# Kernel tuning notes

Hardware: AMD Instinct MI355X
Metric: run time of the kernel (lower is better)

The kernel has to match this reference:

```python
import jax, jax.numpy as jnp
import numpy as np

N_NODES = 50000
N_EDGES = 800000
HIDDEN = 100
NUM_TASKS = 128
NUM_GRAPHS = 2000
ATOM_DIMS = [119, 5, 12, 12, 10, 6, 6, 2, 2]  # OGB full_atom_feature_dims
EPS = 1e-16  # stands in for PyG's clamp(min=0) so that pow(-1) stays finite


def setup_inputs() -> dict:
    key = jax.random.key(0)
    ks = jax.random.split(key, 8)
    x = jax.random.randint(ks[0], (N_NODES, 9), 0, 2, dtype=jnp.int32)
    edge_index = jax.random.randint(ks[1], (2, N_EDGES), 0, N_NODES, dtype=jnp.int32)
    batch = jnp.sort(jax.random.randint(ks[2], (N_NODES,), 0, NUM_GRAPHS, dtype=jnp.int32))
    s = 1.0 / np.sqrt(HIDDEN)
    atom_emb = jax.random.normal(ks[3], (sum(ATOM_DIMS), HIDDEN), jnp.float32)
    W1 = jax.random.normal(ks[4], (HIDDEN, HIDDEN), jnp.float32) * s
    b1 = jnp.zeros((HIDDEN,), jnp.float32)
    W2 = jax.random.normal(ks[5], (HIDDEN, HIDDEN), jnp.float32) * s
    b2 = jnp.zeros((HIDDEN,), jnp.float32)
    Wlin = jax.random.normal(ks[6], (HIDDEN, NUM_TASKS), jnp.float32) * s
    blin = jnp.zeros((NUM_TASKS,), jnp.float32)
    return dict(x=x, edge_index=edge_index, batch=batch, atom_emb=atom_emb,
                W1=W1, b1=b1, W2=W2, b2=b2, Wlin=Wlin, blin=blin)


def reference(x, edge_index, batch, atom_emb, W1, b1, W2, b2, Wlin, blin):
    # --- AtomEncoder: sum of per-feature categorical embeddings ---
    offsets = jnp.asarray(np.concatenate([[0], np.cumsum(ATOM_DIMS)[:-1]]), jnp.int32)
    h = jnp.take(atom_emb, x + offsets[None, :], axis=0).sum(axis=1)  # [N, H]

    # --- GCN normalization with self-loops (gcn_norm, edge_weight=None) ---
    loops = jnp.arange(N_NODES, dtype=edge_index.dtype)
    row = jnp.concatenate([edge_index[0], loops])  # source
    col = jnp.concatenate([edge_index[1], loops])  # target
    ew = jnp.ones(row.shape[0], jnp.float32)
    deg = jax.ops.segment_sum(ew, col, num_segments=N_NODES)  # in-degree incl self-loop
    dinv = jnp.where(deg > 0, deg ** -0.5, 0.0)
    norm = dinv[row] * ew * dinv[col]  # [E+N]
    cnt = jnp.maximum(deg, 1.0)  # messages per target node (for mean)

    def gcn_conv(h, W, b):
        msg = norm[:, None] * (h @ W)[row]  # [E+N, H]
        # PowerMeanAggregation(p=-1): clamp(0,100).pow(-1) -> mean -> clamp(0,100).pow(-1)
        msg = jnp.clip(msg, EPS, 100.0) ** (-1.0)
        agg = jax.ops.segment_sum(msg, col, num_segments=N_NODES) / cnt[:, None]
        return jnp.clip(agg, EPS, 100.0) ** (-1.0) + b

    h = jax.nn.relu(gcn_conv(h, W1, b1))
    h = gcn_conv(h, W2, b2)

    # --- global_mean_pool over batch ---
    gcnt = jax.ops.segment_sum(jnp.ones((N_NODES,), jnp.float32), batch, num_segments=NUM_GRAPHS)
    pooled = jax.ops.segment_sum(h, batch, num_segments=NUM_GRAPHS) / jnp.maximum(gcnt, 1.0)[:, None]

    return pooled @ Wlin + blin  # [NUM_GRAPHS, NUM_TASKS]
```

## Files before the change

### kernel.cpp

```cpp
#include <hip/hip_runtime.h>

#define N_NODES   50000
#define N_EDGES   800000
#define HIDDEN    100
#define NUM_TASKS 128
#define NUM_GRAPHS 2000
#define EPS 1e-16f

static __device__ __forceinline__ float rcp_fast(float v) {
    return __builtin_amdgcn_rcpf(v);
}
static __device__ __forceinline__ float invclip(float v) {
    return rcp_fast(fminf(fmaxf(v, EPS), 100.0f));
}
static __device__ __forceinline__ unsigned pack_bf16x2(float a, float b) {
    unsigned r;
    asm("v_cvt_pk_bf16_f32 %0, %1, %2" : "=v"(r) : "v"(a), "v"(b));
    return r;
}

__global__ void deg_count_kernel(const int* __restrict__ col, int* __restrict__ deg) {
    int e = blockIdx.x * blockDim.x + threadIdx.x;
    if (e < N_EDGES) atomicAdd(&deg[col[e]], 1);
}

__global__ void blk_sum_kernel(const int* __restrict__ deg, int* __restrict__ bsum) {
    int i = blockIdx.x * 256 + threadIdx.x;
    int v = (i < N_NODES) ? deg[i] : 0;
#pragma unroll
    for (int off = 32; off > 0; off >>= 1) v += __shfl_down(v, off, 64);
    __shared__ int ws[4];
    if ((threadIdx.x & 63) == 0) ws[threadIdx.x >> 6] = v;
    __syncthreads();
    if (threadIdx.x == 0) bsum[blockIdx.x] = ws[0] + ws[1] + ws[2] + ws[3];
}

__global__ void bsum_scan_kernel(int* __restrict__ bsum, int nblk) {
    __shared__ int buf[256];
    int t = threadIdx.x;
    int v = (t < nblk) ? bsum[t] : 0;
    buf[t] = v;
    __syncthreads();
    for (int off = 1; off < 256; off <<= 1) {
        int x = (t >= off) ? buf[t - off] : 0;
        __syncthreads();
        buf[t] += x;
        __syncthreads();
    }
    if (t < nblk) bsum[t] = buf[t] - v;
}

__global__ void blk_scan_kernel(const int* __restrict__ deg, const int* __restrict__ bbase,
                                int* __restrict__ csr_off, float* __restrict__ dinv,
                                int* __restrict__ cursor) {
    __shared__ int buf[256];
    int t = threadIdx.x;
    int i = blockIdx.x * 256 + t;
    int dv = (i < N_NODES) ? deg[i] : 0;
    buf[t] = dv;
    __syncthreads();
    for (int off = 1; off < 256; off <<= 1) {
        int x = (t >= off) ? buf[t - off] : 0;
        __syncthreads();
        buf[t] += x;
        __syncthreads();
    }
    if (i < N_NODES) {
        csr_off[i] = bbase[blockIdx.x] + buf[t] - dv;
        dinv[i] = 1.0f / sqrtf((float)(dv + 1));
        cursor[i] = 0;
    } else if (i == N_NODES) {
        csr_off[N_NODES] = N_EDGES;
    }
}

__global__ void scatter_kernel(const int* __restrict__ row, const int* __restrict__ col,
                               const int* __restrict__ csr_off, int* __restrict__ cursor,
                               const float* __restrict__ dinv, int2* __restrict__ csr_pack) {
    int e = blockIdx.x * blockDim.x + threadIdx.x;
    if (e >= N_EDGES) return;
    int s = row[e], d = col[e];
    int pos = csr_off[d] + atomicAdd(&cursor[d], 1);
    int2 p;
    p.x = s;
    p.y = __float_as_int(dinv[s] * dinv[d]);
    csr_pack[pos] = p;
}

__global__ void encoder_kernel(const int* __restrict__ x, const float* __restrict__ emb,
                               float* __restrict__ h) {
    int n = blockIdx.x;
    int d = threadIdx.x;
    if (d >= HIDDEN) return;
    const int offs[9] = {0, 119, 124, 136, 148, 158, 164, 170, 172};
    float acc = 0.0f;
#pragma unroll
    for (int f = 0; f < 9; ++f) {
        int idx = x[n * 9 + f] + offs[f];
        acc += emb[idx * HIDDEN + d];
    }
    h[n * HIDDEN + d] = acc;
}

#define MM_NODES 64
#define WL_PAD   10032
__global__ __launch_bounds__(512) void matmul_kernel(const float* __restrict__ h,
                                                     const float* __restrict__ W,
                                                     unsigned* __restrict__ outb) {
    __shared__ float Wl[WL_PAD];
    __shared__ float hl[MM_NODES * HIDDEN];
    int tid = threadIdx.x;
    int nb = blockIdx.x * MM_NODES;

    for (int i = tid; i < WL_PAD; i += 512)
        Wl[i] = (i < HIDDEN * HIDDEN) ? W[i] : 0.0f;
    for (int i = tid; i < MM_NODES * HIDDEN; i += 512) {
        int n = i / HIDDEN;
        hl[i] = (nb + n < N_NODES) ? h[(size_t)(nb + n) * HIDDEN + (i % HIDDEN)] : 0.0f;
    }
    __syncthreads();

    int tx = tid & 31;
    int ty = tid >> 5;

    float4 acc[4];
#pragma unroll
    for (int jn = 0; jn < 4; ++jn) acc[jn] = make_float4(0.f, 0.f, 0.f, 0.f);

    for (int kk = 0; kk < HIDDEN; kk += 4) {
        float hs[4][4];
#pragma unroll
        for (int jn = 0; jn < 4; ++jn) {
            float4 hv = *(const float4*)&hl[(ty + 16 * jn) * HIDDEN + kk];
            hs[jn][0] = hv.x; hs[jn][1] = hv.y; hs[jn][2] = hv.z; hs[jn][3] = hv.w;
        }
#pragma unroll
        for (int dk = 0; dk < 4; ++dk) {
            float4 wv = *(const float4*)&Wl[(kk + dk) * HIDDEN + 4 * tx];
#pragma unroll
            for (int jn = 0; jn < 4; ++jn) {
                acc[jn].x += hs[jn][dk] * wv.x;
                acc[jn].y += hs[jn][dk] * wv.y;
                acc[jn].z += hs[jn][dk] * wv.z;
                acc[jn].w += hs[jn][dk] * wv.w;
            }
        }
    }

    if (tx < 25) {
#pragma unroll
        for (int jn = 0; jn < 4; ++jn) {
            int n = nb + ty + 16 * jn;
            if (n < N_NODES) {
                uint2 pk;
                pk.x = pack_bf16x2(acc[jn].x, acc[jn].y);
                pk.y = pack_bf16x2(acc[jn].z, acc[jn].w);
                *(uint2*)&outb[(size_t)n * 50 + 2 * tx] = pk;
            }
        }
    }
}

__global__ __launch_bounds__(128) void agg_kernel(
        const unsigned* __restrict__ hw16, const int* __restrict__ csr_off,
        const int2* __restrict__ csr_pack, const float* __restrict__ dinv,
        const int* __restrict__ deg, const float* __restrict__ bias,
        float* __restrict__ out, int relu) {
    int wid  = (blockIdx.x * blockDim.x + threadIdx.x) >> 6;
    int lane = threadIdx.x & 63;
    if (wid >= N_NODES) return;
    int n = wid;
    bool act = lane < 50;

    float cnt = (float)(deg[n] + 1);
    float dn  = dinv[n];
    float nrm = dn * dn;

    float2 acc = make_float2(0.f, 0.f);
    if (act) {
        unsigned u = hw16[(size_t)n * 50 + lane];
        acc.x = invclip(nrm * __int_as_float(u << 16));
        acc.y = invclip(nrm * __int_as_float(u & 0xFFFF0000u));
    }

    int beg = csr_off[n], end = csr_off[n + 1];
    int i = beg;
    for (; i + 4 <= end; i += 4) {
        int2 p0 = csr_pack[i];
        int2 p1 = csr_pack[i + 1];
        int2 p2 = csr_pack[i + 2];
        int2 p3 = csr_pack[i + 3];
        unsigned u0 = act ? hw16[(size_t)p0.x * 50 + lane] : 0u;
        unsigned u1 = act ? hw16[(size_t)p1.x * 50 + lane] : 0u;
        unsigned u2 = act ? hw16[(size_t)p2.x * 50 + lane] : 0u;
        unsigned u3 = act ? hw16[(size_t)p3.x * 50 + lane] : 0u;
        float w0 = __int_as_float(p0.y), w1 = __int_as_float(p1.y);
        float w2 = __int_as_float(p2.y), w3 = __int_as_float(p3.y);
        acc.x += invclip(w0 * __int_as_float(u0 << 16));
        acc.y += invclip(w0 * __int_as_float(u0 & 0xFFFF0000u));
        acc.x += invclip(w1 * __int_as_float(u1 << 16));
        acc.y += invclip(w1 * __int_as_float(u1 & 0xFFFF0000u));
        acc.x += invclip(w2 * __int_as_float(u2 << 16));
        acc.y += invclip(w2 * __int_as_float(u2 & 0xFFFF0000u));
        acc.x += invclip(w3 * __int_as_float(u3 << 16));
        acc.y += invclip(w3 * __int_as_float(u3 & 0xFFFF0000u));
    }
    for (; i < end; ++i) {
        int2 p = csr_pack[i];
        unsigned u = act ? hw16[(size_t)p.x * 50 + lane] : 0u;
        float w = __int_as_float(p.y);
        acc.x += invclip(w * __int_as_float(u << 16));
        acc.y += invclip(w * __int_as_float(u & 0xFFFF0000u));
    }

    if (act) {
        float rcnt = rcp_fast(cnt);
        float2 o;
        o.x = invclip(acc.x * rcnt) + bias[2 * lane];
        o.y = invclip(acc.y * rcnt) + bias[2 * lane + 1];
        if (relu) { o.x = fmaxf(o.x, 0.f); o.y = fmaxf(o.y, 0.f); }
        *(float2*)&out[(size_t)n * HIDDEN + 2 * lane] = o;
    }
}

__global__ void pool_final_kernel(const float* __restrict__ h, const int* __restrict__ batch,
                                  const float* __restrict__ Wlin, const float* __restrict__ blin,
                                  float* __restrict__ out) {
    int g = blockIdx.x;
    int t = threadIdx.x;
    __shared__ float pl[HIDDEN];

    int lo = 0, hi = N_NODES;
    while (lo < hi) { int mid = (lo + hi) >> 1; if (batch[mid] < g) lo = mid + 1; else hi = mid; }
    int start = lo;
    hi = N_NODES;
    while (lo < hi) { int mid = (lo + hi) >> 1; if (batch[mid] < g + 1) lo = mid + 1; else hi = mid; }
    int end = lo;

    float inv = 1.0f / fmaxf((float)(end - start), 1.0f);
    if (t < HIDDEN) {
        float acc = 0.f;
        for (int n = start; n < end; ++n) acc += h[(size_t)n * HIDDEN + t];
        pl[t] = acc * inv;
    }
    __syncthreads();

    float o = 0.f;
#pragma unroll 4
    for (int j = 0; j < HIDDEN; ++j) o += pl[j] * Wlin[j * NUM_TASKS + t];
    out[(size_t)g * NUM_TASKS + t] = o + blin[t];
}

extern "C" void kernel_launch(void* const* d_in, const int* in_sizes, int n_in,
                              void* d_out, int out_size, void* d_ws, size_t ws_size,
                              hipStream_t stream) {
    const int*   x     = (const int*)d_in[0];
    const int*   ei    = (const int*)d_in[1];
    const int*   batch = (const int*)d_in[2];
    const float* emb   = (const float*)d_in[3];
    const float* W1    = (const float*)d_in[4];
    const float* b1    = (const float*)d_in[5];
    const float* W2    = (const float*)d_in[6];
    const float* b2    = (const float*)d_in[7];
    const float* Wlin  = (const float*)d_in[8];
    const float* blin  = (const float*)d_in[9];
    float* out = (float*)d_out;

    const int* row = ei;
    const int* col = ei + N_EDGES;

    char* ws = (char*)d_ws;
    auto alloc = [&](size_t bytes) -> char* {
        char* p = ws;
        ws += (bytes + 255) & ~(size_t)255;
        return p;
    };
    int*      deg      = (int*)     alloc((size_t)N_NODES * 4);
    int*      cursor   = (int*)     alloc((size_t)N_NODES * 4);
    int*      csr_off  = (int*)     alloc((size_t)(N_NODES + 1) * 4);
    float*    dinv     = (float*)   alloc((size_t)N_NODES * 4);
    int2*     csr_pack = (int2*)    alloc((size_t)N_EDGES * 8);
    float*    bufA     = (float*)   alloc((size_t)N_NODES * HIDDEN * 4);
    unsigned* hw16     = (unsigned*)alloc((size_t)N_NODES * 50 * 4);
    int*      bsum     = (int*)     alloc(256 * 4);

    const int SCAN_BLOCKS = (N_NODES + 255) / 256;

    hipMemsetAsync(deg, 0, (size_t)N_NODES * 4, stream);
    deg_count_kernel<<<(N_EDGES + 255) / 256, 256, 0, stream>>>(col, deg);
    blk_sum_kernel<<<SCAN_BLOCKS, 256, 0, stream>>>(deg, bsum);
    bsum_scan_kernel<<<1, 256, 0, stream>>>(bsum, SCAN_BLOCKS);
    blk_scan_kernel<<<SCAN_BLOCKS, 256, 0, stream>>>(deg, bsum, csr_off, dinv, cursor);
    scatter_kernel<<<(N_EDGES + 255) / 256, 256, 0, stream>>>(row, col, csr_off, cursor, dinv,
                                                              csr_pack);
    encoder_kernel<<<N_NODES, 128, 0, stream>>>(x, emb, bufA);

    const int MM_BLOCKS = (N_NODES + MM_NODES - 1) / MM_NODES;
    matmul_kernel<<<MM_BLOCKS, 512, 0, stream>>>(bufA, W1, hw16);
    agg_kernel<<<(N_NODES + 1) / 2, 128, 0, stream>>>(hw16, csr_off, csr_pack,
                                                      dinv, deg, b1, bufA, 1);
    matmul_kernel<<<MM_BLOCKS, 512, 0, stream>>>(bufA, W2, hw16);
    agg_kernel<<<(N_NODES + 1) / 2, 128, 0, stream>>>(hw16, csr_off, csr_pack,
                                                      dinv, deg, b2, bufA, 0);

    pool_final_kernel<<<NUM_GRAPHS, 128, 0, stream>>>(bufA, batch, Wlin, blin, out);
}
```

Before: 317.5 us.

## Process two nodes per wavefront in aggregation with 8-byte bf16 gathers

The aggregation kernel now maps two destination nodes onto each 64-lane wavefront, one per half-wave. Each of 25 active lanes per half loads a uint2 holding four bf16 features, so 50 of 64 lanes do work instead of 50 of 64 with 4-byte loads. The goal is fewer wavefronts, wider memory transactions and better lane use. The cost is divergence: the edge loop runs until both halves finish, so the wave follows the higher-degree node, and out-of-range neighbour slots load clamped indices.

```diff
diff --git a/kernel.cpp b/kernel.cpp
--- a/kernel.cpp
+++ b/kernel.cpp
@@ -18,6 +18,8 @@
     asm("v_cvt_pk_bf16_f32 %0, %1, %2" : "=v"(r) : "v"(a), "v"(b));
     return r;
 }
+static __device__ __forceinline__ float bf_lo(unsigned u) { return __int_as_float(u << 16); }
+static __device__ __forceinline__ float bf_hi(unsigned u) { return __int_as_float(u & 0xFFFF0000u); }
 
 __global__ void deg_count_kernel(const int* __restrict__ col, int* __restrict__ deg) {
     int e = blockIdx.x * blockDim.x + threadIdx.x;
@@ -161,65 +163,67 @@
     }
 }
 
-__global__ __launch_bounds__(128) void agg_kernel(
+__global__ __launch_bounds__(256) void agg_kernel(
         const unsigned* __restrict__ hw16, const int* __restrict__ csr_off,
         const int2* __restrict__ csr_pack, const float* __restrict__ dinv,
         const int* __restrict__ deg, const float* __restrict__ bias,
         float* __restrict__ out, int relu) {
     int wid  = (blockIdx.x * blockDim.x + threadIdx.x) >> 6;
     int lane = threadIdx.x & 63;
-    if (wid >= N_NODES) return;
-    int n = wid;
-    bool act = lane < 50;
+    if (wid >= (N_NODES + 1) / 2) return;
+    int half = lane >> 5;
+    int q    = lane & 31;
+    int n    = 2 * wid + half;
+    bool act = q < 25;
+
+    const uint2* hw2 = (const uint2*)hw16;
 
     float cnt = (float)(deg[n] + 1);
     float dn  = dinv[n];
     float nrm = dn * dn;
 
-    float2 acc = make_float2(0.f, 0.f);
+    float a0 = 0.f, a1 = 0.f, a2 = 0.f, a3 = 0.f;
     if (act) {
-        unsigned u = hw16[(size_t)n * 50 + lane];
-        acc.x = invclip(nrm * __int_as_float(u << 16));
-        acc.y = invclip(nrm * __int_as_float(u & 0xFFFF0000u));
-    }
-
-    int beg = csr_off[n], end = csr_off[n + 1];
-    int i = beg;
-    for (; i + 4 <= end; i += 4) {
-        int2 p0 = csr_pack[i];
-        int2 p1 = csr_pack[i + 1];
-        int2 p2 = csr_pack[i + 2];
-        int2 p3 = csr_pack[i + 3];
-        unsigned u0 = act ? hw16[(size_t)p0.x * 50 + lane] : 0u;
-        unsigned u1 = act ? hw16[(size_t)p1.x * 50 + lane] : 0u;
-        unsigned u2 = act ? hw16[(size_t)p2.x * 50 + lane] : 0u;
-        unsigned u3 = act ? hw16[(size_t)p3.x * 50 + lane] : 0u;
-        float w0 = __int_as_float(p0.y), w1 = __int_as_float(p1.y);
-        float w2 = __int_as_float(p2.y), w3 = __int_as_float(p3.y);
-        acc.x += invclip(w0 * __int_as_float(u0 << 16));
-        acc.y += invclip(w0 * __int_as_float(u0 & 0xFFFF0000u));
-        acc.x += invclip(w1 * __int_as_float(u1 << 16));
-        acc.y += invclip(w1 * __int_as_float(u1 & 0xFFFF0000u));
-        acc.x += invclip(w2 * __int_as_float(u2 << 16));
-        acc.y += invclip(w2 * __int_as_float(u2 & 0xFFFF0000u));
-        acc.x += invclip(w3 * __int_as_float(u3 << 16));
-        acc.y += invclip(w3 * __int_as_float(u3 & 0xFFFF0000u));
-    }
-    for (; i < end; ++i) {
-        int2 p = csr_pack[i];
-        unsigned u = act ? hw16[(size_t)p.x * 50 + lane] : 0u;
-        float w = __int_as_float(p.y);
-        acc.x += invclip(w * __int_as_float(u << 16));
-        acc.y += invclip(w * __int_as_float(u & 0xFFFF0000u));
+        uint2 u = hw2[(size_t)n * 25 + q];
+        a0 = invclip(nrm * bf_lo(u.x)); a1 = invclip(nrm * bf_hi(u.x));
+        a2 = invclip(nrm * bf_lo(u.y)); a3 = invclip(nrm * bf_hi(u.y));
+    }
+
+    int beg = csr_off[n];
+    int len = csr_off[n + 1] - beg;
+
+    const long long* packs = (const long long*)csr_pack;
+    for (int k = 0; __any(k < len); k += 4) {
+#pragma unroll
+        for (int j = 0; j < 4; ++j) {
+            int kk = k + j;
+            bool on = kk < len;
+            int idx = beg + (on ? kk : (len > 0 ? len - 1 : 0));
+            idx = (idx < N_EDGES) ? idx : (N_EDGES - 1);
+            long long qp = packs[idx];
+            int   src = (int)qp;
+            float w   = __int_as_float((int)(qp >> 32));
+            if (on & act) {
+                uint2 u = hw2[(size_t)src * 25 + q];
+                a0 += invclip(w * bf_lo(u.x)); a1 += invclip(w * bf_hi(u.x));
+                a2 += invclip(w * bf_lo(u.y)); a3 += invclip(w * bf_hi(u.y));
+            }
+        }
     }
 
     if (act) {
         float rcnt = rcp_fast(cnt);
-        float2 o;
-        o.x = invclip(acc.x * rcnt) + bias[2 * lane];
-        o.y = invclip(acc.y * rcnt) + bias[2 * lane + 1];
-        if (relu) { o.x = fmaxf(o.x, 0.f); o.y = fmaxf(o.y, 0.f); }
-        *(float2*)&out[(size_t)n * HIDDEN + 2 * lane] = o;
+        float4 bv = *(const float4*)&bias[4 * q];
+        float4 o;
+        o.x = invclip(a0 * rcnt) + bv.x;
+        o.y = invclip(a1 * rcnt) + bv.y;
+        o.z = invclip(a2 * rcnt) + bv.z;
+        o.w = invclip(a3 * rcnt) + bv.w;
+        if (relu) {
+            o.x = fmaxf(o.x, 0.f); o.y = fmaxf(o.y, 0.f);
+            o.z = fmaxf(o.z, 0.f); o.w = fmaxf(o.w, 0.f);
+        }
+        *(float4*)&out[(size_t)n * HIDDEN + 4 * q] = o;
     }
 }
 
@@ -295,13 +299,16 @@
                                                               csr_pack);
     encoder_kernel<<<N_NODES, 128, 0, stream>>>(x, emb, bufA);
 
-    const int MM_BLOCKS = (N_NODES + MM_NODES - 1) / MM_NODES;
+    const int MM_BLOCKS  = (N_NODES + MM_NODES - 1) / MM_NODES;
+    const int AGG_WAVES  = (N_NODES + 1) / 2;
+    const int AGG_BLOCKS = (AGG_WAVES + 3) / 4;
+
     matmul_kernel<<<MM_BLOCKS, 512, 0, stream>>>(bufA, W1, hw16);
-    agg_kernel<<<(N_NODES + 1) / 2, 128, 0, stream>>>(hw16, csr_off, csr_pack,
-                                                      dinv, deg, b1, bufA, 1);
+    agg_kernel<<<AGG_BLOCKS, 256, 0, stream>>>(hw16, csr_off, csr_pack,
+                                               dinv, deg, b1, bufA, 1);
     matmul_kernel<<<MM_BLOCKS, 512, 0, stream>>>(bufA, W2, hw16);
-    agg_kernel<<<(N_NODES + 1) / 2, 128, 0, stream>>>(hw16, csr_off, csr_pack,
-                                                      dinv, deg, b2, bufA, 0);
+    agg_kernel<<<AGG_BLOCKS, 256, 0, stream>>>(hw16, csr_off, csr_pack,
+                                               dinv, deg, b2, bufA, 0);
 
     pool_final_kernel<<<NUM_GRAPHS, 128, 0, stream>>>(bufA, batch, Wlin, blin, out);
 }
```

After: 324.2 us. +2.1%, slower.
